# Optimization experiments

Measured on AMD Instinct MI355X. Metric: run time of the kernel, lower is better.

The kernel has to match this reference:

```python
import jax, jax.numpy as jnp
import numpy as np
from jax import lax

OBS_LEN = 20
N_COORD = 2
HIDDEN = 192  # z_dim + s_dim = 128 + 64
N = 131072


def setup_inputs() -> dict:
    key = jax.random.key(0)
    ks = jax.random.split(key, 6)
    obs_traj_rel = jax.random.normal(ks[0], (OBS_LEN, N, N_COORD), dtype=jnp.float32)
    pred_lstm_hidden = jax.random.normal(ks[1], (N, HIDDEN), dtype=jnp.float32)
    # LSTMCell params (torch layout: weight_ih [4H, in], weight_hh [4H, H])
    w_ih = jax.random.normal(ks[2], (4 * HIDDEN, N_COORD), dtype=jnp.float32) * 0.1
    w_hh = jax.random.normal(ks[3], (4 * HIDDEN, HIDDEN), dtype=jnp.float32) * 0.1
    b_ih = jnp.zeros((4 * HIDDEN,), dtype=jnp.float32)
    b_hh = jnp.zeros((4 * HIDDEN,), dtype=jnp.float32)
    # hidden2pos Linear
    w_out = jax.random.normal(ks[4], (N_COORD, HIDDEN), dtype=jnp.float32) * 0.1
    b_out = jnp.zeros((N_COORD,), dtype=jnp.float32)
    return {
        "obs_traj_rel": obs_traj_rel,
        "pred_lstm_hidden": pred_lstm_hidden,
        "w_ih": w_ih,
        "w_hh": w_hh,
        "b_ih": b_ih,
        "b_hh": b_hh,
        "w_out": w_out,
        "b_out": b_out,
    }


def reference(obs_traj_rel, pred_lstm_hidden, w_ih, w_hh, b_ih, b_hh, w_out, b_out):
    T = obs_traj_rel.shape[0]
    # step i uses obs_traj_rel[max(i-1, 0)] -> indices [0, 0, 1, ..., T-2]
    idx = jnp.concatenate([jnp.zeros((1,), jnp.int32), jnp.arange(T - 1, dtype=jnp.int32)])
    xs = obs_traj_rel[idx, :, :N_COORD]  # [T, N, 2]

    def step(carry, x_t):
        h, c = carry
        gates = x_t @ w_ih.T + b_ih + h @ w_hh.T + b_hh  # [N, 4H]
        i, f, g, o = jnp.split(gates, 4, axis=-1)  # torch LSTMCell gate order
        i = jax.nn.sigmoid(i)
        f = jax.nn.sigmoid(f)
        g = jnp.tanh(g)
        o = jax.nn.sigmoid(o)
        c_new = f * c + i * g
        h_new = o * jnp.tanh(c_new)
        out = h_new @ w_out.T + b_out  # [N, 2]
        return (h_new, c_new), out

    c0 = jnp.zeros_like(pred_lstm_hidden)
    (_, _), outs = lax.scan(step, (pred_lstm_hidden, c0), xs)
    return outs  # [T, N, 2]
```

## Files before the change

### kernel.cpp

```cpp
#include <hip/hip_runtime.h>

typedef _Float16 half8 __attribute__((ext_vector_type(8)));
typedef float floatx4 __attribute__((ext_vector_type(4)));

#define T_STEPS 20
#define NSEQ 131072
#define HID 192
#define ROWS 32
#define HPAD 200
#define HROWS 17
#define WOFF 147456
#define XOFF 150528
#define FR_TOTAL (XOFF + 6144)

__device__ __forceinline__ float fsig(float x) {
    return __builtin_amdgcn_rcpf(1.f + __builtin_amdgcn_exp2f(-1.4426950408889634f * x));
}
__device__ __forceinline__ float ftanh(float x) {
    return 1.f - 2.f * __builtin_amdgcn_rcpf(__builtin_amdgcn_exp2f(2.8853900817779268f * x) + 1.f);
}

__global__ void build_frags(const float* __restrict__ whh,
                            const float* __restrict__ wout,
                            const float* __restrict__ wih,
                            const float* __restrict__ bih,
                            const float* __restrict__ bhh,
                            _Float16* __restrict__ dst) {
    int i = blockIdx.x * 256 + threadIdx.x;
    if (i < WOFF) {
        int e = i & 7, L = (i >> 3) & 63, g = (i >> 9) & 3, u = i >> 11;
        int kc = u % 6, ht = u / 6;
        int n = L & 15, q = L >> 4;
        dst[i] = (_Float16)whh[(size_t)(g * HID + ht * 16 + n) * HID + kc * 32 + q * 8 + e];
    } else if (i < XOFF) {
        int k = i - WOFF;
        int e = k & 7, L = (k >> 3) & 63, kc = k >> 9;
        int n = L & 15, q = L >> 4;
        dst[i] = (_Float16)((n < 2) ? wout[n * HID + kc * 32 + q * 8 + e] : 0.f);
    } else if (i < FR_TOTAL) {
        int k = i - XOFF;
        int e = k & 7, n = (k >> 3) & 15, g = (k >> 7) & 3, ht = k >> 9;
        int col = g * HID + ht * 16 + n;
        float v = 0.f;
        if (e == 0)      v = wih[col * 2];
        else if (e == 1) v = wih[col * 2 + 1];
        else if (e == 2) v = bih[col] + bhh[col];
        dst[i] = (_Float16)v;
    }
}

__global__ __launch_bounds__(768, 3) void lstm_fused_kernel(
    const float* __restrict__ obs,
    const float* __restrict__ h0,
    const float* __restrict__ b_out,
    const _Float16* __restrict__ frags,
    float* __restrict__ out)
{
    __shared__ _Float16 h0b[2][HROWS][HPAD];
    __shared__ _Float16 h1b[HROWS][HPAD];
    __shared__ _Float16 b_lds[49152];
    __shared__ _Float16 wo_lds[3072];
    __shared__ _Float16 wx_lds[6144];
    __shared__ _Float16 wxz[512];
    __shared__ float2 x_all[T_STEPS][ROWS];

    const int tid  = threadIdx.x;
    const int wave = tid >> 6;
    const int lane = tid & 63;
    const int quad = lane >> 4;
    const int l16  = lane & 15;
    const int ht   = wave;
    const int base = blockIdx.x * ROWS;
    const int j    = ht * 16 + l16;

    half8 bw[16];
#pragma unroll
    for (int kc = 0; kc < 4; ++kc)
#pragma unroll
        for (int g = 0; g < 4; ++g)
            bw[kc * 4 + g] = *(const half8*)&frags[(((ht * 6 + kc) * 4 + g) << 9) + lane * 8];

    const half8 HZ = {0, 0, 0, 0, 0, 0, 0, 0};
    for (int i = tid; i < 2 * HROWS * HPAD / 8; i += 768) ((half8*)h0b)[i] = HZ;
    for (int i = tid; i < HROWS * HPAD / 8; i += 768)     ((half8*)h1b)[i] = HZ;
    for (int i = tid; i < 6144; i += 768) {
        int g = (i >> 6) & 3, u = i >> 8, k2 = u & 1, h = u >> 1;
        ((half8*)b_lds)[i] = *(const half8*)&frags[(((h * 6 + 4 + k2) * 4 + g) << 9) + (i & 63) * 8];
    }
    if (tid < 384) ((half8*)wo_lds)[tid] = *(const half8*)&frags[WOFF + tid * 8];
    ((half8*)wx_lds)[tid] = *(const half8*)&frags[XOFF + tid * 8];
    if (tid < 64) ((half8*)wxz)[tid] = HZ;
    if (tid < T_STEPS * ROWS) {
        int t = tid >> 5, r = tid & 31;
        int src = (t == 0) ? 0 : (t - 1);
        x_all[t][r] = *(const float2*)&obs[((size_t)src * NSEQ + base + r) * 2];
    }
    __syncthreads();

    for (int i = tid; i < ROWS * HID / 4; i += 768) {
        float4 v = *(const float4*)&h0[(size_t)base * HID + i * 4];
        int row = (i * 4) / HID, k = i * 4 - row * HID;
        _Float16* d = (row < 16) ? &h0b[0][row][k] : &h1b[row - 16][k];
        d[0] = (_Float16)v.x; d[1] = (_Float16)v.y;
        d[2] = (_Float16)v.z; d[3] = (_Float16)v.w;
    }
    if (tid < 64) {
        int row = tid >> 1;
        _Float16 v = (_Float16)((const float*)x_all[0])[tid];
        if (row < 16) h0b[0][row][192 + (tid & 1)] = v;
        else          h1b[row - 16][192 + (tid & 1)] = v;
    }
    if (tid < 16)      { h0b[0][tid][194] = (_Float16)1.f; h0b[1][tid][194] = (_Float16)1.f; }
    else if (tid < 32)   h1b[tid - 16][194] = (_Float16)1.f;
    __syncthreads();

    const float bo_n = (l16 < 2) ? b_out[l16] : 0.f;
    const _Float16* wxp = (quad == 0) ? (wx_lds + ht * 512 + l16 * 8) : wxz;

    float c[8];
#pragma unroll
    for (int i = 0; i < 8; ++i) c[i] = 0.f;

    auto run_mfma = [&](const _Float16* hb, floatx4* acc) {
        const _Float16* ar = hb + l16 * HPAD;
        half8 ax = *(const half8*)(ar + 192 + quad * 8);
#pragma unroll
        for (int g = 0; g < 4; ++g) {
            half8 bxg = *(const half8*)(wxp + g * 128);
            acc[g] = __builtin_amdgcn_mfma_f32_16x16x32_f16(ax, bxg, acc[g], 0, 0, 0);
        }
#pragma unroll
        for (int kc = 0; kc < 4; ++kc) {
            half8 a = *(const half8*)(ar + kc * 32 + quad * 8);
#pragma unroll
            for (int g = 0; g < 4; ++g)
                acc[g] = __builtin_amdgcn_mfma_f32_16x16x32_f16(a, bw[kc * 4 + g], acc[g], 0, 0, 0);
        }
#pragma unroll
        for (int k2 = 0; k2 < 2; ++k2) {
            half8 a = *(const half8*)(ar + (4 + k2) * 32 + quad * 8);
#pragma unroll
            for (int g = 0; g < 4; ++g) {
                half8 b = *(const half8*)&b_lds[(((ht * 2 + k2) * 4 + g) << 9) + lane * 8];
                acc[g] = __builtin_amdgcn_mfma_f32_16x16x32_f16(a, b, acc[g], 0, 0, 0);
            }
        }
    };

    auto activation = [&](floatx4* acc, _Float16* hw, int cb) {
#pragma unroll
        for (int r = 0; r < 4; ++r) {
            const int row = quad * 4 + r;
            const float cn = fsig(acc[1][r]) * c[cb + r]
                           + fsig(acc[0][r]) * ftanh(acc[2][r]);
            c[cb + r] = cn;
            hw[row * HPAD + j] = (_Float16)(fsig(acc[3][r]) * ftanh(cn));
        }
    };

    auto run_wout = [&](int ot, const _Float16* hbl, const _Float16* hbh) {
#pragma unroll
        for (int rt = 0; rt < 2; ++rt) {
            const _Float16* ar = ((rt == 0) ? hbl : hbh) + l16 * HPAD;
            floatx4 ao = {bo_n, bo_n, bo_n, bo_n};
#pragma unroll
            for (int kc = 0; kc < 6; ++kc) {
                half8 a = *(const half8*)(ar + kc * 32 + quad * 8);
                half8 b = *(const half8*)&wo_lds[kc * 512 + lane * 8];
                ao = __builtin_amdgcn_mfma_f32_16x16x32_f16(a, b, ao, 0, 0, 0);
            }
            if (l16 < 2) {
#pragma unroll
                for (int r = 0; r < 4; ++r)
                    out[((size_t)ot * NSEQ + base + rt * 16 + quad * 4 + r) * 2 + l16] = ao[r];
            }
        }
    };

    floatx4 accA[4], accB[4];
#pragma unroll
    for (int g = 0; g < 4; ++g) accA[g] = (floatx4){0.f, 0.f, 0.f, 0.f};
    run_mfma(&h0b[0][0][0], accA);

    for (int t = 0; t < T_STEPS; ++t) {
#pragma unroll
        for (int g = 0; g < 4; ++g) accB[g] = (floatx4){0.f, 0.f, 0.f, 0.f};
        run_mfma(&h1b[0][0], accB);
        if (ht == 0 && t > 0)
            run_wout(t - 1, &h0b[t & 1][0][0], &h1b[0][0]);
        activation(accA, &h0b[(t + 1) & 1][0][0], 0);
        if (ht == 11 && lane < 32 && t < T_STEPS - 1)
            h0b[(t + 1) & 1][lane >> 1][192 + (lane & 1)] =
                (_Float16)((const float*)x_all[t + 1])[lane];
        __syncthreads();

        if (t < T_STEPS - 1) {
#pragma unroll
            for (int g = 0; g < 4; ++g) accA[g] = (floatx4){0.f, 0.f, 0.f, 0.f};
            run_mfma(&h0b[(t + 1) & 1][0][0], accA);
        }
        activation(accB, &h1b[0][0], 4);
        if (ht == 11 && lane < 32 && t < T_STEPS - 1)
            h1b[lane >> 1][192 + (lane & 1)] =
                (_Float16)((const float*)x_all[t + 1])[32 + lane];
        __syncthreads();
    }

    if (ht == 0)
        run_wout(T_STEPS - 1, &h0b[0][0][0], &h1b[0][0]);
}

extern "C" void kernel_launch(void* const* d_in, const int* in_sizes, int n_in,
                              void* d_out, int out_size, void* d_ws, size_t ws_size,
                              hipStream_t stream) {
    const float* obs  = (const float*)d_in[0];
    const float* h0   = (const float*)d_in[1];
    const float* wih  = (const float*)d_in[2];
    const float* whh  = (const float*)d_in[3];
    const float* bih  = (const float*)d_in[4];
    const float* bhh  = (const float*)d_in[5];
    const float* wout = (const float*)d_in[6];
    const float* bout = (const float*)d_in[7];
    float* out = (float*)d_out;
    _Float16* frags = (_Float16*)d_ws;

    build_frags<<<(FR_TOTAL + 255) / 256, 256, 0, stream>>>(whh, wout, wih, bih, bhh, frags);
    lstm_fused_kernel<<<NSEQ / ROWS, 768, 0, stream>>>(obs, h0, bout, frags, out);
}
```

Before: 1.291 ms.

## Interleave MFMA with activation via sched_group_barrier and fuse gate math

Moves the input-projection weight fragments from LDS into registers. The LSTM gate activations are rewritten to share reciprocals: one rcp produces the new cell value and one produces the hidden value, instead of separate sigmoids and tanhs. Explicit sched_group_barrier patterns interleave the MFMA, LDS reads and VALU work of the next half-tile's gate GEMM with the current half's activation. The output projection is split across two waves and the last timestep is peeled out of the loop. The aim is to overlap MFMA and transcendental latency and to cut LDS traffic, at the cost of more register pressure and a rigid schedule hint.

Measured after the change: 1.190 ms. -7.8%, faster.

```diff
diff --git a/kernel.cpp b/kernel.cpp
--- a/kernel.cpp
+++ b/kernel.cpp
@@ -13,12 +13,7 @@
 #define XOFF 150528
 #define FR_TOTAL (XOFF + 6144)
 
-__device__ __forceinline__ float fsig(float x) {
-    return __builtin_amdgcn_rcpf(1.f + __builtin_amdgcn_exp2f(-1.4426950408889634f * x));
-}
-__device__ __forceinline__ float ftanh(float x) {
-    return 1.f - 2.f * __builtin_amdgcn_rcpf(__builtin_amdgcn_exp2f(2.8853900817779268f * x) + 1.f);
-}
+#define MFMA16(a, b, c) __builtin_amdgcn_mfma_f32_16x16x32_f16((a), (b), (c), 0, 0, 0)
 
 __global__ void build_frags(const float* __restrict__ whh,
                             const float* __restrict__ wout,
@@ -49,7 +44,8 @@
     }
 }
 
-__global__ __launch_bounds__(768, 3) void lstm_fused_kernel(
+__global__ __launch_bounds__(768) __attribute__((amdgpu_waves_per_eu(3, 3)))
+void lstm_fused_kernel(
     const float* __restrict__ obs,
     const float* __restrict__ h0,
     const float* __restrict__ b_out,
@@ -60,8 +56,6 @@
     __shared__ _Float16 h1b[HROWS][HPAD];
     __shared__ _Float16 b_lds[49152];
     __shared__ _Float16 wo_lds[3072];
-    __shared__ _Float16 wx_lds[6144];
-    __shared__ _Float16 wxz[512];
     __shared__ float2 x_all[T_STEPS][ROWS];
 
     const int tid  = threadIdx.x;
@@ -73,14 +67,20 @@
     const int base = blockIdx.x * ROWS;
     const int j    = ht * 16 + l16;
 
-    half8 bw[16];
+    const half8 HZ = {0, 0, 0, 0, 0, 0, 0, 0};
+
+    half8 bw[16], bx[4];
 #pragma unroll
     for (int kc = 0; kc < 4; ++kc)
 #pragma unroll
         for (int g = 0; g < 4; ++g)
             bw[kc * 4 + g] = *(const half8*)&frags[(((ht * 6 + kc) * 4 + g) << 9) + lane * 8];
-
-    const half8 HZ = {0, 0, 0, 0, 0, 0, 0, 0};
+#pragma unroll
+    for (int g = 0; g < 4; ++g)
+        bx[g] = (quad == 0)
+              ? *(const half8*)&frags[XOFF + ht * 512 + g * 128 + l16 * 8]
+              : HZ;
+
     for (int i = tid; i < 2 * HROWS * HPAD / 8; i += 768) ((half8*)h0b)[i] = HZ;
     for (int i = tid; i < HROWS * HPAD / 8; i += 768)     ((half8*)h1b)[i] = HZ;
     for (int i = tid; i < 6144; i += 768) {
@@ -88,8 +88,6 @@
         ((half8*)b_lds)[i] = *(const half8*)&frags[(((h * 6 + 4 + k2) * 4 + g) << 9) + (i & 63) * 8];
     }
     if (tid < 384) ((half8*)wo_lds)[tid] = *(const half8*)&frags[WOFF + tid * 8];
-    ((half8*)wx_lds)[tid] = *(const half8*)&frags[XOFF + tid * 8];
-    if (tid < 64) ((half8*)wxz)[tid] = HZ;
     if (tid < T_STEPS * ROWS) {
         int t = tid >> 5, r = tid & 31;
         int src = (t == 0) ? 0 : (t - 1);
@@ -115,99 +113,119 @@
     __syncthreads();
 
     const float bo_n = (l16 < 2) ? b_out[l16] : 0.f;
-    const _Float16* wxp = (quad == 0) ? (wx_lds + ht * 512 + l16 * 8) : wxz;
 
     float c[8];
 #pragma unroll
     for (int i = 0; i < 8; ++i) c[i] = 0.f;
 
-    auto run_mfma = [&](const _Float16* hb, floatx4* acc) {
+    auto build = [&](const _Float16* hb, floatx4* aN) {
         const _Float16* ar = hb + l16 * HPAD;
+        const _Float16* blp = b_lds;
+        asm volatile("" : "+v"(blp));
+#pragma unroll
+        for (int g = 0; g < 4; ++g) aN[g] = (floatx4){0.f, 0.f, 0.f, 0.f};
         half8 ax = *(const half8*)(ar + 192 + quad * 8);
 #pragma unroll
-        for (int g = 0; g < 4; ++g) {
-            half8 bxg = *(const half8*)(wxp + g * 128);
-            acc[g] = __builtin_amdgcn_mfma_f32_16x16x32_f16(ax, bxg, acc[g], 0, 0, 0);
-        }
+        for (int g = 0; g < 4; ++g)
+            aN[g] = MFMA16(ax, bx[g], aN[g]);
 #pragma unroll
         for (int kc = 0; kc < 4; ++kc) {
             half8 a = *(const half8*)(ar + kc * 32 + quad * 8);
 #pragma unroll
             for (int g = 0; g < 4; ++g)
-                acc[g] = __builtin_amdgcn_mfma_f32_16x16x32_f16(a, bw[kc * 4 + g], acc[g], 0, 0, 0);
+                aN[g] = MFMA16(a, bw[kc * 4 + g], aN[g]);
         }
 #pragma unroll
         for (int k2 = 0; k2 < 2; ++k2) {
             half8 a = *(const half8*)(ar + (4 + k2) * 32 + quad * 8);
 #pragma unroll
             for (int g = 0; g < 4; ++g) {
-                half8 b = *(const half8*)&b_lds[(((ht * 2 + k2) * 4 + g) << 9) + lane * 8];
-                acc[g] = __builtin_amdgcn_mfma_f32_16x16x32_f16(a, b, acc[g], 0, 0, 0);
+                half8 b = *(const half8*)&blp[(((ht * 2 + k2) * 4 + g) << 9) + lane * 8];
+                aN[g] = MFMA16(a, b, aN[g]);
             }
         }
     };
 
-    auto activation = [&](floatx4* acc, _Float16* hw, int cb) {
+    auto act = [&](floatx4* aO, _Float16* hw, int cb) {
 #pragma unroll
         for (int r = 0; r < 4; ++r) {
             const int row = quad * 4 + r;
-            const float cn = fsig(acc[1][r]) * c[cb + r]
-                           + fsig(acc[0][r]) * ftanh(acc[2][r]);
+            const float Ai = __builtin_amdgcn_exp2f(-1.4426950408889634f * aO[0][r]);
+            const float Af = __builtin_amdgcn_exp2f(-1.4426950408889634f * aO[1][r]);
+            const float Bg = __builtin_amdgcn_exp2f( 2.8853900817779268f * aO[2][r]);
+            const float Co = __builtin_amdgcn_exp2f(-1.4426950408889634f * aO[3][r]);
+            const float Qf = 1.f + Af;
+            const float Pg = (1.f + Ai) * (Bg + 1.f);
+            const float Nn = c[cb + r] * Pg + Qf * (Bg - 1.f);
+            const float cn = Nn * __builtin_amdgcn_rcpf(Qf * Pg);
             c[cb + r] = cn;
-            hw[row * HPAD + j] = (_Float16)(fsig(acc[3][r]) * ftanh(cn));
-        }
-    };
-
-    auto run_wout = [&](int ot, const _Float16* hbl, const _Float16* hbh) {
-#pragma unroll
-        for (int rt = 0; rt < 2; ++rt) {
-            const _Float16* ar = ((rt == 0) ? hbl : hbh) + l16 * HPAD;
-            floatx4 ao = {bo_n, bo_n, bo_n, bo_n};
-#pragma unroll
-            for (int kc = 0; kc < 6; ++kc) {
-                half8 a = *(const half8*)(ar + kc * 32 + quad * 8);
-                half8 b = *(const half8*)&wo_lds[kc * 512 + lane * 8];
-                ao = __builtin_amdgcn_mfma_f32_16x16x32_f16(a, b, ao, 0, 0, 0);
-            }
-            if (l16 < 2) {
-#pragma unroll
-                for (int r = 0; r < 4; ++r)
-                    out[((size_t)ot * NSEQ + base + rt * 16 + quad * 4 + r) * 2 + l16] = ao[r];
-            }
+            const float Dc = __builtin_amdgcn_exp2f(2.8853900817779268f * cn);
+            const float hv = (Dc - 1.f) * __builtin_amdgcn_rcpf((1.f + Co) * (Dc + 1.f));
+            hw[row * HPAD + j] = (_Float16)hv;
+        }
+    };
+
+    auto sched_pattern = [&]() {
+#pragma unroll
+        for (int u = 0; u < 7; ++u) {
+            __builtin_amdgcn_sched_group_barrier(0x100, 2, 0);
+            __builtin_amdgcn_sched_group_barrier(0x008, 4, 0);
+            __builtin_amdgcn_sched_group_barrier(0x002, 16, 0);
+        }
+        __builtin_amdgcn_sched_group_barrier(0x200, 4, 0);
+    };
+
+    auto wout1 = [&](int ot, const _Float16* hbase) {
+        const _Float16* ar = hbase + l16 * HPAD;
+        floatx4 ao = {bo_n, bo_n, bo_n, bo_n};
+#pragma unroll
+        for (int kc = 0; kc < 6; ++kc) {
+            half8 a = *(const half8*)(ar + kc * 32 + quad * 8);
+            half8 b = *(const half8*)&wo_lds[kc * 512 + lane * 8];
+            ao = MFMA16(a, b, ao);
+        }
+        if (l16 < 2) {
+#pragma unroll
+            for (int r = 0; r < 4; ++r)
+                out[((size_t)ot * NSEQ + base + ht * 16 + quad * 4 + r) * 2 + l16] = ao[r];
         }
     };
 
     floatx4 accA[4], accB[4];
-#pragma unroll
-    for (int g = 0; g < 4; ++g) accA[g] = (floatx4){0.f, 0.f, 0.f, 0.f};
-    run_mfma(&h0b[0][0][0], accA);
-
-    for (int t = 0; t < T_STEPS; ++t) {
-#pragma unroll
-        for (int g = 0; g < 4; ++g) accB[g] = (floatx4){0.f, 0.f, 0.f, 0.f};
-        run_mfma(&h1b[0][0], accB);
-        if (ht == 0 && t > 0)
-            run_wout(t - 1, &h0b[t & 1][0][0], &h1b[0][0]);
-        activation(accA, &h0b[(t + 1) & 1][0][0], 0);
-        if (ht == 11 && lane < 32 && t < T_STEPS - 1)
-            h0b[(t + 1) & 1][lane >> 1][192 + (lane & 1)] =
+    build(&h0b[0][0][0], accA);
+
+    for (int t = 0; t < T_STEPS - 1; ++t) {
+        _Float16* h0n = &h0b[(t + 1) & 1][0][0];
+
+        build(&h1b[0][0], accB);
+        act(accA, h0n, 0);
+        sched_pattern();
+        if (ht < 2 && t > 0)
+            wout1(t - 1, (ht == 0) ? &h0b[t & 1][0][0] : &h1b[0][0]);
+        if (ht == 11 && lane < 32)
+            h0n[(lane >> 1) * HPAD + 192 + (lane & 1)] =
                 (_Float16)((const float*)x_all[t + 1])[lane];
         __syncthreads();
 
-        if (t < T_STEPS - 1) {
-#pragma unroll
-            for (int g = 0; g < 4; ++g) accA[g] = (floatx4){0.f, 0.f, 0.f, 0.f};
-            run_mfma(&h0b[(t + 1) & 1][0][0], accA);
-        }
-        activation(accB, &h1b[0][0], 4);
-        if (ht == 11 && lane < 32 && t < T_STEPS - 1)
+        build(h0n, accA);
+        act(accB, &h1b[0][0], 4);
+        sched_pattern();
+        if (ht == 11 && lane < 32)
             h1b[lane >> 1][192 + (lane & 1)] =
                 (_Float16)((const float*)x_all[t + 1])[32 + lane];
         __syncthreads();
     }
 
-    if (ht == 0)
-        run_wout(T_STEPS - 1, &h0b[0][0][0], &h1b[0][0]);
+    build(&h1b[0][0], accB);
+    act(accA, &h0b[0][0][0], 0);
+    sched_pattern();
+    if (ht < 2)
+        wout1(18, (ht == 0) ? &h0b[1][0][0] : &h1b[0][0]);
+    __syncthreads();
+    act(accB, &h1b[0][0], 4);
+    __syncthreads();
+    if (ht < 2)
+        wout1(19, (ht == 0) ? &h0b[0][0][0] : &h1b[0][0]);
 }
 
 extern "C" void kernel_launch(void* const* d_in, const int* in_sizes, int n_in,
```
